# Kernel tuning notes

Measured on AMD Instinct MI355X. Metric: run time of the kernel, lower is better.

The kernel has to match this reference:

```python
import jax, jax.numpy as jnp
import numpy as np

B, OUT, IN = 4096, 1024, 1024
BN_EPS = 1e-5


def setup_inputs() -> dict:
    key = jax.random.key(0)
    kx, k1, k2, k3 = jax.random.split(key, 4)
    # kaiming_uniform_ with a=sqrt(5): bound = sqrt(6 / ((1+a^2) * fan_in)) = 1/sqrt(fan_in)
    bound = 1.0 / np.sqrt(IN)
    x = jax.random.normal(kx, (B, IN), dtype=jnp.float32)
    c1 = jax.random.uniform(k1, (OUT, IN), jnp.float32, -bound, bound)
    c2 = jax.random.uniform(k2, (OUT, IN), jnp.float32, -bound, bound)
    c3 = jax.random.uniform(k3, (OUT, IN), jnp.float32, -bound, bound)
    bias = jnp.zeros((OUT, IN), jnp.float32)
    gamma = jnp.ones((OUT,), jnp.float32)   # BatchNorm1d weight
    beta = jnp.zeros((OUT,), jnp.float32)   # BatchNorm1d bias
    return {"x": x, "c1": c1, "c2": c2, "c3": c3, "bias": bias,
            "gamma": gamma, "beta": beta}


def reference(x, c1, c2, c3, bias, gamma, beta):
    # Fused polynomial 'matmul': out[b,o] = sum_i x*c1 + x^2*c2 + x^3*c3 + bias
    x2 = x * x
    x3 = x2 * x
    y = (jnp.einsum('bi,oi->bo', x, c1)
         + jnp.einsum('bi,oi->bo', x2, c2)
         + jnp.einsum('bi,oi->bo', x3, c3)
         + jnp.sum(bias, axis=1))  # bias reduced over in_features
    # BatchNorm1d (training mode: batch statistics, biased variance)
    mean = jnp.mean(y, axis=0)
    var = jnp.var(y, axis=0)
    return (y - mean) * jax.lax.rsqrt(var + BN_EPS) * gamma + beta
```

## Files before the change

### kernel.cpp

```cpp
#include <hip/hip_runtime.h>
#include <stdint.h>

#define B_ROWS 4096
#define OUTF   1024
#define INF    1024
#define KTOT   3072
#define BN_EPS 1e-5f
#define BM 128
#define BN 128
#define BK 64
#define NSTEP (KTOT / BK)

typedef short  short8  __attribute__((ext_vector_type(8)));
typedef float  floatx4 __attribute__((ext_vector_type(4)));

struct alignas(8) s4 { short x, y, z, w; };

#define WAIT_VM8 0x0F78
#define WAIT_VM4 0x0F74
#define WAIT_VM0 0x0F70

__device__ __forceinline__ short f2bf(float f) {
  union { float f; uint32_t u; } cv; cv.f = f;
  uint32_t u = cv.u;
  uint32_t r = (u + 0x7fffu + ((u >> 16) & 1u)) >> 16;
  return (short)r;
}

__device__ __forceinline__ void load_lds16(const void* g, void* l) {
  __builtin_amdgcn_global_load_lds(
      (const __attribute__((address_space(1))) uint32_t*)(uintptr_t)g,
      (__attribute__((address_space(3))) uint32_t*)(uint32_t)(uintptr_t)l,
      16, 0, 0);
}

__global__ void prep_all(const float4* __restrict__ x4,
                         const float4* __restrict__ c1, const float4* __restrict__ c2,
                         const float4* __restrict__ c3,
                         short* __restrict__ Xb, short* __restrict__ Wb) {
  int b = blockIdx.x;
  if (b < 4096) {
    int idx = b * 256 + threadIdx.x;
    float4 v = x4[idx];
    int row = idx >> 8;
    int c   = (idx & 255) << 2;
    size_t base = (size_t)row * KTOT + c;
    s4 p1 = { f2bf(v.x), f2bf(v.y), f2bf(v.z), f2bf(v.w) };
    float ax = v.x * v.x, ay = v.y * v.y, az = v.z * v.z, aw = v.w * v.w;
    s4 p2 = { f2bf(ax), f2bf(ay), f2bf(az), f2bf(aw) };
    s4 p3 = { f2bf(ax * v.x), f2bf(ay * v.y), f2bf(az * v.z), f2bf(aw * v.w) };
    *(s4*)&Xb[base]        = p1;
    *(s4*)&Xb[base + 1024] = p2;
    *(s4*)&Xb[base + 2048] = p3;
  } else {
    int idx = (b - 4096) * 256 + threadIdx.x;
    int row = idx >> 8;
    int c   = (idx & 255) << 2;
    size_t base = (size_t)row * KTOT + c;
    float4 a = c1[idx], bb = c2[idx], d = c3[idx];
    s4 p1 = { f2bf(a.x),  f2bf(a.y),  f2bf(a.z),  f2bf(a.w)  };
    s4 p2 = { f2bf(bb.x), f2bf(bb.y), f2bf(bb.z), f2bf(bb.w) };
    s4 p3 = { f2bf(d.x),  f2bf(d.y),  f2bf(d.z),  f2bf(d.w)  };
    *(s4*)&Wb[base]        = p1;
    *(s4*)&Wb[base + 1024] = p2;
    *(s4*)&Wb[base + 2048] = p3;
  }
}

__global__ __launch_bounds__(512, 2) void gemm_poly(
    const short* __restrict__ Xb, const short* __restrict__ Wb,
    float* __restrict__ Y, float* __restrict__ psum, float* __restrict__ psq) {
  __shared__ __align__(16) short As[4][BM * BK];
  __shared__ __align__(16) short Bs[4][BN * BK];
  const int tid  = threadIdx.x;
  const int lane = tid & 63;
  const int wave = tid >> 6;
  const int wr = wave >> 2;
  const int wc = wave & 3;
  const int lb  = blockIdx.x;
  const int xcd = lb & 7;
  const int sl  = lb >> 3;
  const int bx  = sl & 7;
  const int by  = xcd * 4 + (sl >> 3);
  const int row0 = by * BM;
  const int col0 = bx * BN;
  const short* Ag = Xb + (size_t)row0 * KTOT;
  const short* Bg = Wb + (size_t)col0 * KTOT;
  const int frag_m = lane & 15;
  const int sel = lane >> 4;
  floatx4 acc[4][2] = {};

  int off01[2];
  #pragma unroll
  for (int i = 0; i < 2; ++i) {
    int c = tid + i * 512;
    int r = c >> 3, p = c & 7;
    int lg = p ^ (r & 7);
    off01[i] = r * KTOT + lg * 8;
  }

  #pragma unroll
  for (int t = 0; t < 3; ++t) {
    #pragma unroll
    for (int i = 0; i < 2; ++i) {
      load_lds16(Ag + off01[i] + t * BK, &As[t][(tid + i * 512) * 8]);
      load_lds16(Bg + off01[i] + t * BK, &Bs[t][(tid + i * 512) * 8]);
    }
  }

#define GSTEP(CUR, PRE, KT_PRE, DO_PRE, WAITIMM)                              \
  {                                                                           \
    __builtin_amdgcn_s_waitcnt(WAITIMM);                                      \
    __builtin_amdgcn_s_barrier();                                             \
    if (DO_PRE) {                                                             \
      _Pragma("unroll")                                                       \
      for (int i = 0; i < 2; ++i) {                                           \
        load_lds16(Ag + off01[i] + (KT_PRE), &As[PRE][(tid + i * 512) * 8]);  \
        load_lds16(Bg + off01[i] + (KT_PRE), &Bs[PRE][(tid + i * 512) * 8]);  \
      }                                                                       \
    }                                                                         \
    _Pragma("unroll")                                                         \
    for (int s = 0; s < 2; ++s) {                                             \
      short8 af[4], bfr[2];                                                   \
      _Pragma("unroll")                                                       \
      for (int i = 0; i < 4; ++i) {                                           \
        int r = wr * 64 + i * 16 + frag_m;                                    \
        int p = (s * 4 + sel) ^ (r & 7);                                      \
        af[i] = *(const short8*)&As[CUR][r * BK + p * 8];                     \
      }                                                                       \
      _Pragma("unroll")                                                       \
      for (int j = 0; j < 2; ++j) {                                           \
        int r = wc * 32 + j * 16 + frag_m;                                    \
        int p = (s * 4 + sel) ^ (r & 7);                                      \
        bfr[j] = *(const short8*)&Bs[CUR][r * BK + p * 8];                    \
      }                                                                       \
      _Pragma("unroll")                                                       \
      for (int i = 0; i < 4; ++i)                                             \
        _Pragma("unroll")                                                     \
        for (int j = 0; j < 2; ++j)                                           \
          acc[i][j] = __builtin_amdgcn_mfma_f32_16x16x32_bf16(                \
              af[i], bfr[j], acc[i][j], 0, 0, 0);                             \
    }                                                                         \
  }

  for (int t4 = 0; t4 < 44; t4 += 4) {
    GSTEP(0, 3, (t4 + 3) * BK, 1, WAIT_VM8);
    GSTEP(1, 0, (t4 + 4) * BK, 1, WAIT_VM8);
    GSTEP(2, 1, (t4 + 5) * BK, 1, WAIT_VM8);
    GSTEP(3, 2, (t4 + 6) * BK, 1, WAIT_VM8);
  }
  GSTEP(0, 3, 47 * BK, 1, WAIT_VM8);
  GSTEP(1, 0, 0, 0, WAIT_VM8);
  GSTEP(2, 0, 0, 0, WAIT_VM4);
  GSTEP(3, 0, 0, 0, WAIT_VM0);
#undef GSTEP

  float* colred = (float*)&As[0][0];
  float sv[2] = {0.f, 0.f}, sq[2] = {0.f, 0.f};
  #pragma unroll
  for (int j = 0; j < 2; ++j)
    #pragma unroll
    for (int i = 0; i < 4; ++i)
      #pragma unroll
      for (int r = 0; r < 4; ++r) {
        float v = acc[i][j][r];
        sv[j] += v; sq[j] += v * v;
      }
  #pragma unroll
  for (int j = 0; j < 2; ++j) {
    sv[j] += __shfl_xor(sv[j], 16, 64); sv[j] += __shfl_xor(sv[j], 32, 64);
    sq[j] += __shfl_xor(sq[j], 16, 64); sq[j] += __shfl_xor(sq[j], 32, 64);
  }
  if (sel == 0) {
    #pragma unroll
    for (int j = 0; j < 2; ++j) {
      int cc = wc * 32 + j * 16 + frag_m;
      colred[wr * 256 + cc]       = sv[j];
      colred[wr * 256 + 128 + cc] = sq[j];
    }
  }
  const int drow = sel << 2;
  #pragma unroll
  for (int j = 0; j < 2; ++j) {
    int gc = col0 + wc * 32 + j * 16 + frag_m;
    #pragma unroll
    for (int i = 0; i < 4; ++i) {
      int gr = row0 + wr * 64 + i * 16 + drow;
      #pragma unroll
      for (int r = 0; r < 4; ++r)
        Y[(size_t)(gr + r) * OUTF + gc] = acc[i][j][r];
    }
  }
  __syncthreads();
  if (tid < BN) {
    psum[(size_t)by * OUTF + col0 + tid] = colred[tid]       + colred[256 + tid];
    psq [(size_t)by * OUTF + col0 + tid] = colred[128 + tid] + colred[384 + tid];
  }
}

__global__ void bn_fused(const float* __restrict__ psum, const float* __restrict__ psq,
                         const float* __restrict__ gamma, const float* __restrict__ beta,
                         float* __restrict__ Y) {
  __shared__ float sc[32], sh[32];
  const int c0 = blockIdx.x * 32;
  const int t = threadIdx.x;
  if (t < 32) {
    float s = 0.f, s2 = 0.f;
    #pragma unroll 8
    for (int p = 0; p < 32; ++p) {
      s  += psum[p * OUTF + c0 + t];
      s2 += psq [p * OUTF + c0 + t];
    }
    float mean = s * (1.0f / B_ROWS);
    float var  = s2 * (1.0f / B_ROWS) - mean * mean;
    float scale = gamma[c0 + t] * rsqrtf(var + BN_EPS);
    sc[t] = scale;
    sh[t] = beta[c0 + t] - mean * scale;
  }
  __syncthreads();
  const int f4c = t & 7;
  const int rr  = t >> 3;
  const int row0 = blockIdx.y * 256;
  float4* Y4 = (float4*)Y;
  const int cb = f4c * 4;
  float s0 = sc[cb], s1 = sc[cb+1], s2 = sc[cb+2], s3 = sc[cb+3];
  float h0 = sh[cb], h1 = sh[cb+1], h2 = sh[cb+2], h3 = sh[cb+3];
  #pragma unroll
  for (int it = 0; it < 8; ++it) {
    int row = row0 + it * 32 + rr;
    size_t idx = (size_t)row * 256 + (c0 >> 2) + f4c;
    float4 v = Y4[idx];
    v.x = v.x * s0 + h0; v.y = v.y * s1 + h1;
    v.z = v.z * s2 + h2; v.w = v.w * s3 + h3;
    Y4[idx] = v;
  }
}

extern "C" void kernel_launch(void* const* d_in, const int* in_sizes, int n_in,
                              void* d_out, int out_size, void* d_ws, size_t ws_size,
                              hipStream_t stream) {
  const float* x     = (const float*)d_in[0];
  const float* c1    = (const float*)d_in[1];
  const float* c2    = (const float*)d_in[2];
  const float* c3    = (const float*)d_in[3];
  const float* gamma = (const float*)d_in[5];
  const float* beta  = (const float*)d_in[6];
  float* out = (float*)d_out;
  char* ws = (char*)d_ws;

  short* Xb   = (short*)(ws);
  short* Wb   = (short*)(ws + 25165824);
  float* psum = (float*)(ws + 31457280);
  float* psq  = (float*)(ws + 31588352);

  prep_all<<<5120, 256, 0, stream>>>((const float4*)x, (const float4*)c1,
                                     (const float4*)c2, (const float4*)c3,
                                     Xb, Wb);

  gemm_poly<<<256, 512, 0, stream>>>(Xb, Wb, out, psum, psq);

  dim3 bgrid(OUTF / 32, B_ROWS / 256);
  bn_fused<<<bgrid, 256, 0, stream>>>(psum, psq, gamma, beta, out);
}
```

Before: 125.4 us.

## Compute x squared and cubed in-register inside GEMM instead of materializing them

Result: slower. 137.6 us (+9.7%).

```diff
diff --git a/kernel.cpp b/kernel.cpp
--- a/kernel.cpp
+++ b/kernel.cpp
@@ -4,12 +4,12 @@
 #define B_ROWS 4096
 #define OUTF   1024
 #define INF    1024
-#define KTOT   3072
+#define KX     1024
 #define BN_EPS 1e-5f
 #define BM 128
 #define BN 128
-#define BK 64
-#define NSTEP (KTOT / BK)
+#define BK 32
+#define NSTEP (KX / BK)
 
 typedef short  short8  __attribute__((ext_vector_type(8)));
 typedef float  floatx4 __attribute__((ext_vector_type(4)));
@@ -32,6 +32,27 @@
       (const __attribute__((address_space(1))) uint32_t*)(uintptr_t)g,
       (__attribute__((address_space(3))) uint32_t*)(uint32_t)(uintptr_t)l,
       16, 0, 0);
+}
+
+__device__ __forceinline__ uint32_t pack2(float hi, float lo) {
+  union { float f; uint32_t u; } H, L; H.f = hi; L.f = lo;
+  return ((H.u + 0x8000u) & 0xffff0000u) | ((L.u + 0x8000u) >> 16);
+}
+
+__device__ __forceinline__ void frag_pows(const short8 a, short8* a2, short8* a3) {
+  const uint32_t* ap = (const uint32_t*)&a;
+  uint32_t* p2 = (uint32_t*)a2;
+  uint32_t* p3 = (uint32_t*)a3;
+  #pragma unroll
+  for (int h = 0; h < 4; ++h) {
+    uint32_t u = ap[h];
+    union { uint32_t u; float f; } lo, hi;
+    lo.u = u << 16; hi.u = u & 0xffff0000u;
+    float l2 = lo.f * lo.f, h2 = hi.f * hi.f;
+    float l3 = l2 * lo.f,  h3 = h2 * hi.f;
+    p2[h] = pack2(h2, l2);
+    p3[h] = pack2(h3, l3);
+  }
 }
 
 __global__ void prep_all(const float4* __restrict__ x4,
@@ -44,26 +65,20 @@
     float4 v = x4[idx];
     int row = idx >> 8;
     int c   = (idx & 255) << 2;
-    size_t base = (size_t)row * KTOT + c;
     s4 p1 = { f2bf(v.x), f2bf(v.y), f2bf(v.z), f2bf(v.w) };
-    float ax = v.x * v.x, ay = v.y * v.y, az = v.z * v.z, aw = v.w * v.w;
-    s4 p2 = { f2bf(ax), f2bf(ay), f2bf(az), f2bf(aw) };
-    s4 p3 = { f2bf(ax * v.x), f2bf(ay * v.y), f2bf(az * v.z), f2bf(aw * v.w) };
-    *(s4*)&Xb[base]        = p1;
-    *(s4*)&Xb[base + 1024] = p2;
-    *(s4*)&Xb[base + 2048] = p3;
+    *(s4*)&Xb[(size_t)row * KX + c] = p1;
   } else {
     int idx = (b - 4096) * 256 + threadIdx.x;
     int row = idx >> 8;
     int c   = (idx & 255) << 2;
-    size_t base = (size_t)row * KTOT + c;
+    size_t base = (size_t)row * KX + c;
     float4 a = c1[idx], bb = c2[idx], d = c3[idx];
     s4 p1 = { f2bf(a.x),  f2bf(a.y),  f2bf(a.z),  f2bf(a.w)  };
     s4 p2 = { f2bf(bb.x), f2bf(bb.y), f2bf(bb.z), f2bf(bb.w) };
     s4 p3 = { f2bf(d.x),  f2bf(d.y),  f2bf(d.z),  f2bf(d.w)  };
-    *(s4*)&Wb[base]        = p1;
-    *(s4*)&Wb[base + 1024] = p2;
-    *(s4*)&Wb[base + 2048] = p3;
+    *(s4*)&Wb[base]           = p1;
+    *(s4*)&Wb[base + 1048576] = p2;
+    *(s4*)&Wb[base + 2097152] = p3;
   }
 }
 
@@ -71,7 +86,7 @@
     const short* __restrict__ Xb, const short* __restrict__ Wb,
     float* __restrict__ Y, float* __restrict__ psum, float* __restrict__ psq) {
   __shared__ __align__(16) short As[4][BM * BK];
-  __shared__ __align__(16) short Bs[4][BN * BK];
+  __shared__ __align__(16) short Bs[4][3 * BN * BK];
   const int tid  = threadIdx.x;
   const int lane = tid & 63;
   const int wave = tid >> 6;
@@ -84,28 +99,22 @@
   const int by  = xcd * 4 + (sl >> 3);
   const int row0 = by * BM;
   const int col0 = bx * BN;
-  const short* Ag = Xb + (size_t)row0 * KTOT;
-  const short* Bg = Wb + (size_t)col0 * KTOT;
   const int frag_m = lane & 15;
   const int sel = lane >> 4;
   floatx4 acc[4][2] = {};
 
-  int off01[2];
-  #pragma unroll
-  for (int i = 0; i < 2; ++i) {
-    int c = tid + i * 512;
-    int r = c >> 3, p = c & 7;
-    int lg = p ^ (r & 7);
-    off01[i] = r * KTOT + lg * 8;
-  }
+  const int r_  = tid >> 2;
+  const int l_  = (tid & 3) ^ ((r_ >> 1) & 3);
+  const int aoff = (row0 + r_) * KX + l_ * 8;
+  const size_t boff = (size_t)(col0 + r_) * KX + l_ * 8;
+  const int ldst = tid * 8;
 
   #pragma unroll
   for (int t = 0; t < 3; ++t) {
-    #pragma unroll
-    for (int i = 0; i < 2; ++i) {
-      load_lds16(Ag + off01[i] + t * BK, &As[t][(tid + i * 512) * 8]);
-      load_lds16(Bg + off01[i] + t * BK, &Bs[t][(tid + i * 512) * 8]);
-    }
+    load_lds16(Xb + aoff + t * BK, &As[t][ldst]);
+    #pragma unroll
+    for (int pi = 0; pi < 3; ++pi)
+      load_lds16(Wb + boff + pi * 1048576 + t * BK, &Bs[t][pi * 4096 + ldst]);
   }
 
 #define GSTEP(CUR, PRE, KT_PRE, DO_PRE, WAITIMM)                              \
@@ -113,43 +122,48 @@
     __builtin_amdgcn_s_waitcnt(WAITIMM);                                      \
     __builtin_amdgcn_s_barrier();                                             \
     if (DO_PRE) {                                                             \
+      load_lds16(Xb + aoff + (KT_PRE), &As[PRE][ldst]);                       \
       _Pragma("unroll")                                                       \
-      for (int i = 0; i < 2; ++i) {                                           \
-        load_lds16(Ag + off01[i] + (KT_PRE), &As[PRE][(tid + i * 512) * 8]);  \
-        load_lds16(Bg + off01[i] + (KT_PRE), &Bs[PRE][(tid + i * 512) * 8]);  \
-      }                                                                       \
+      for (int pi = 0; pi < 3; ++pi)                                          \
+        load_lds16(Wb + boff + pi * 1048576 + (KT_PRE),                       \
+                   &Bs[PRE][pi * 4096 + ldst]);                               \
+    }                                                                         \
+    short8 af[4], af2[4], af3[4], bfr[3][2];                                  \
+    _Pragma("unroll")                                                         \
+    for (int i = 0; i < 4; ++i) {                                             \
+      int r = wr * 64 + i * 16 + frag_m;                                      \
+      int q = sel ^ ((r >> 1) & 3);                                           \
+      af[i] = *(const short8*)&As[CUR][r * BK + q * 8];                       \
+      frag_pows(af[i], &af2[i], &af3[i]);                                     \
     }                                                                         \
     _Pragma("unroll")                                                         \
-    for (int s = 0; s < 2; ++s) {                                             \
-      short8 af[4], bfr[2];                                                   \
-      _Pragma("unroll")                                                       \
-      for (int i = 0; i < 4; ++i) {                                           \
-        int r = wr * 64 + i * 16 + frag_m;                                    \
-        int p = (s * 4 + sel) ^ (r & 7);                                      \
-        af[i] = *(const short8*)&As[CUR][r * BK + p * 8];                     \
-      }                                                                       \
+    for (int pi = 0; pi < 3; ++pi)                                            \
       _Pragma("unroll")                                                       \
       for (int j = 0; j < 2; ++j) {                                           \
         int r = wc * 32 + j * 16 + frag_m;                                    \
-        int p = (s * 4 + sel) ^ (r & 7);                                      \
-        bfr[j] = *(const short8*)&Bs[CUR][r * BK + p * 8];                    \
+        int q = sel ^ ((r >> 1) & 3);                                         \
+        bfr[pi][j] = *(const short8*)&Bs[CUR][pi * 4096 + r * BK + q * 8];    \
       }                                                                       \
+    _Pragma("unroll")                                                         \
+    for (int i = 0; i < 4; ++i)                                               \
       _Pragma("unroll")                                                       \
-      for (int i = 0; i < 4; ++i)                                             \
-        _Pragma("unroll")                                                     \
-        for (int j = 0; j < 2; ++j)                                           \
-          acc[i][j] = __builtin_amdgcn_mfma_f32_16x16x32_bf16(                \
-              af[i], bfr[j], acc[i][j], 0, 0, 0);                             \
-    }                                                                         \
-  }
-
-  for (int t4 = 0; t4 < 44; t4 += 4) {
+      for (int j = 0; j < 2; ++j) {                                           \
+        acc[i][j] = __builtin_amdgcn_mfma_f32_16x16x32_bf16(                  \
+            af[i],  bfr[0][j], acc[i][j], 0, 0, 0);                           \
+        acc[i][j] = __builtin_amdgcn_mfma_f32_16x16x32_bf16(                  \
+            af2[i], bfr[1][j], acc[i][j], 0, 0, 0);                           \
+        acc[i][j] = __builtin_amdgcn_mfma_f32_16x16x32_bf16(                  \
+            af3[i], bfr[2][j], acc[i][j], 0, 0, 0);                           \
+      }                                                                       \
+  }
+
+  for (int t4 = 0; t4 < 28; t4 += 4) {
     GSTEP(0, 3, (t4 + 3) * BK, 1, WAIT_VM8);
     GSTEP(1, 0, (t4 + 4) * BK, 1, WAIT_VM8);
     GSTEP(2, 1, (t4 + 5) * BK, 1, WAIT_VM8);
     GSTEP(3, 2, (t4 + 6) * BK, 1, WAIT_VM8);
   }
-  GSTEP(0, 3, 47 * BK, 1, WAIT_VM8);
+  GSTEP(0, 3, 31 * BK, 1, WAIT_VM8);
   GSTEP(1, 0, 0, 0, WAIT_VM8);
   GSTEP(2, 0, 0, 0, WAIT_VM4);
   GSTEP(3, 0, 0, 0, WAIT_VM0);
@@ -249,9 +263,9 @@
   char* ws = (char*)d_ws;
 
   short* Xb   = (short*)(ws);
-  short* Wb   = (short*)(ws + 25165824);
-  float* psum = (float*)(ws + 31457280);
-  float* psq  = (float*)(ws + 31588352);
+  short* Wb   = (short*)(ws + 8388608);
+  float* psum = (float*)(ws + 14680064);
+  float* psq  = (float*)(ws + 14811136);
 
   prep_all<<<5120, 256, 0, stream>>>((const float4*)x, (const float4*)c1,
                                      (const float4*)c2, (const float4*)c3,
```
